# Kernel optimization log

Hardware: AMD Instinct MI355X
Metric: run time of the kernel (lower is better)

## Reference

```python
import jax, jax.numpy as jnp
import numpy as np


def _conv(x, k, pad):
    # x: NHWC, k: HWIO
    return jax.lax.conv_general_dilated(x, k, (1, 1), pad,
                                        dimension_numbers=('NHWC', 'HWIO', 'NHWC'))


def _hard_sigmoid(z):
    return jnp.clip(0.2 * z + 0.5, 0.0, 1.0)


def _convlstm(x_seq, Wx, Wh, b, return_sequences):
    # x_seq: (B,T,H,W,C); Wx: (5,5,C,4F) VALID; Wh: (5,5,F,4F) SAME; b: (4F,)
    B, T, H, W, C = x_seq.shape
    F4 = Wx.shape[-1]
    F = F4 // 4
    # input-to-state convs for all timesteps in one batched conv
    xz = _conv(x_seq.reshape(B * T, H, W, C), Wx, 'VALID') + b
    Ho, Wo = xz.shape[1], xz.shape[2]
    xz = xz.reshape(B, T, Ho, Wo, F4).transpose(1, 0, 2, 3, 4)  # time-major
    h0 = jnp.zeros((B, Ho, Wo, F), x_seq.dtype)
    c0 = h0

    def step(carry, xt):
        h, c = carry
        z = xt + _conv(h, Wh, 'SAME')
        zi, zf, zc, zo = jnp.split(z, 4, axis=-1)  # keras gate order i,f,c,o
        i = _hard_sigmoid(zi)
        f = _hard_sigmoid(zf)
        o = _hard_sigmoid(zo)
        c = f * c + i * jnp.tanh(zc)
        h = o * jnp.tanh(c)
        return (h, c), (h if return_sequences else None)

    (h, c), hs = jax.lax.scan(step, (h0, c0), xz)
    if return_sequences:
        return hs.transpose(1, 0, 2, 3, 4)  # back to (B,T,Ho,Wo,F)
    return h


def setup_inputs() -> dict:
    key = jax.random.key(0)
    ks = jax.random.split(key, 12)
    B, T, H, W, C = 16, 6, 64, 64, 5

    def p(k, shape, scale=0.05):
        return jax.random.normal(k, shape, dtype=jnp.float32) * scale

    x = jax.random.normal(ks[0], (B, T, H, W, C), dtype=jnp.float32)
    # layer1: Cin=5 -> F=128
    Wx1 = p(ks[1], (5, 5, 5, 512));   Wh1 = p(ks[2], (5, 5, 128, 512));  b1 = jnp.zeros((512,), jnp.float32)
    # layer2: Cin=128 -> F=64
    Wx2 = p(ks[3], (5, 5, 128, 256)); Wh2 = p(ks[4], (5, 5, 64, 256));   b2 = jnp.zeros((256,), jnp.float32)
    # layer3: Cin=64 -> F=64
    Wx3 = p(ks[5], (5, 5, 64, 256));  Wh3 = p(ks[6], (5, 5, 64, 256));   b3 = jnp.zeros((256,), jnp.float32)
    D = 52 * 52 * 64  # 173056 after three valid 5x5 convs
    Wd1 = p(ks[7], (D, 1024), 0.01);  bd1 = jnp.zeros((1024,), jnp.float32)
    Wd2 = p(ks[8], (1024, 1024));     bd2 = jnp.zeros((1024,), jnp.float32)
    Wd3 = p(ks[9], (1024, 4));        bd3 = jnp.zeros((4,), jnp.float32)
    return dict(x=x, Wx1=Wx1, Wh1=Wh1, b1=b1, Wx2=Wx2, Wh2=Wh2, b2=b2,
                Wx3=Wx3, Wh3=Wh3, b3=b3, Wd1=Wd1, bd1=bd1, Wd2=Wd2, bd2=bd2,
                Wd3=Wd3, bd3=bd3)


def reference(x, Wx1, Wh1, b1, Wx2, Wh2, b2, Wx3, Wh3, b3,
              Wd1, bd1, Wd2, bd2, Wd3, bd3):
    # NOTE: the original call() computes an average-pool of the input but then
    # overwrites it with conv1(inputs); the pooled branch is dead code.
    h = _convlstm(x, Wx1, Wh1, b1, True)   # (B,T,60,60,128)
    h = _convlstm(h, Wx2, Wh2, b2, True)   # (B,T,56,56,64)
    h = _convlstm(h, Wx3, Wh3, b3, False)  # (B,52,52,64)
    z = h.reshape(h.shape[0], -1)          # keras Flatten = row-major H,W,C
    z = jax.nn.relu(z @ Wd1 + bd1)
    z = jax.nn.relu(z @ Wd2 + bd2)
    return z @ Wd3 + bd3                   # (B,4)
```

## Files before the change

### kernel.cpp

```cpp
#include <hip/hip_runtime.h>

typedef __bf16 bf16;
typedef bf16 bf16x8 __attribute__((ext_vector_type(8)));
typedef float f32x4 __attribute__((ext_vector_type(4)));

__device__ inline bf16x8 bzero8() {
  bf16x8 v;
#pragma unroll
  for (int i = 0; i < 8; ++i) v[i] = (bf16)0.f;
  return v;
}

__device__ __forceinline__ void gload_lds16(const bf16* g, bf16* l) {
  __builtin_amdgcn_global_load_lds(
      (const __attribute__((address_space(1))) void*)g,
      (__attribute__((address_space(3))) void*)l, 16, 0, 0);
}

#define MFMA16 __builtin_amdgcn_mfma_f32_16x16x32_bf16
#define LGKM0 asm volatile("s_waitcnt lgkmcnt(0)")
#define VMC2 asm volatile("s_waitcnt vmcnt(2)")
#define VMC0 asm volatile("s_waitcnt vmcnt(0)")

template <int CIN, int LOG2C>
__global__ void __launch_bounds__(512, 2)
conv_gemm256(const bf16* __restrict__ in, const bf16* __restrict__ wt,
             const float* __restrict__ bias, const bf16* __restrict__ xz,
             bf16* __restrict__ out_bf, float* __restrict__ out_f,
             int HoWo, int Wo, int inH, int inW,
             int T, int t, int N, int K, int epi)
{
  __shared__ bf16 As[2][2][8192];
  __shared__ bf16 Bs[2][2][8192];

  const int tid  = threadIdx.x;
  const int w    = tid >> 6;
  const int lane = tid & 63;

  const int gx  = gridDim.x;
  const int nwg = gx * gridDim.y;
  int flat = blockIdx.y * gx + blockIdx.x;
  {
    const int xcd = flat & 7, o = flat >> 3;
    const int qq = nwg >> 3, rr = nwg & 7;
    flat = (xcd < rr ? xcd * (qq + 1) : rr * (qq + 1) + (xcd - rr) * qq) + o;
  }
  const int n0 = (flat % gx) << 8;
  const int m0 = (flat / gx) << 8;

  const long inHW = (long)inH * inW;
  const int lr8  = lane >> 3;
  const int koff = ((lane & 7) ^ lr8) << 3;

  long baseA[2][2];
  const bf16* wrowp[2][2];
#pragma unroll
  for (int h = 0; h < 2; ++h)
#pragma unroll
    for (int j = 0; j < 2; ++j) {
      const int row = ((j * 8 + w) << 3) + lr8;
      const int gm  = m0 + h * 128 + row;
      const int img = gm / HoWo;
      const int p   = gm - img * HoWo;
      const int ay  = p / Wo;
      const int ax  = p - ay * Wo;
      baseA[h][j] = ((long)img * inHW + (long)ay * inW + ax) << LOG2C;
      wrowp[h][j] = wt + (long)(n0 + h * 128 + row) * K + koff;
    }

  const int KT = K >> 6;

  auto stage = [&](int kt, int half) {
    if (kt >= KT) return;
    const int slot = kt & 1;
    if (half < 2) {
      const int kk = kt << 6;
      const int kc = kk >> LOG2C;
      const int ky = kc / 5;
      const int kx = kc - ky * 5;
      const long toff = ((long)(ky * inW + kx) << LOG2C) + (kk & (CIN - 1)) + koff;
      bf16* d = &As[slot][half][w << 9];
      gload_lds16(in + baseA[half][0] + toff, d);
      gload_lds16(in + baseA[half][1] + toff, d + 4096);
    } else {
      const int h = half - 2;
      bf16* d = &Bs[slot][h][w << 9];
      gload_lds16(wrowp[h][0] + (kt << 6), d);
      gload_lds16(wrowp[h][1] + (kt << 6), d + 4096);
    }
  };

  const int lrow = lane & 15;
  const int lq   = lane >> 4;
  const int wm   = w >> 2;
  const int wn   = w & 3;
  const int s7   = lrow & 7;

  auto rdA = [&](int slot, int r, int ks) -> bf16x8 {
    const int row = (r << 4) + lrow;
    const int ch  = ((ks << 2) + lq) ^ s7;
    return *(const bf16x8*)&As[slot][wm][(row << 6) + (ch << 3)];
  };
  auto rdB = [&](int slot, int cq, int ks) -> bf16x8 {
    const int row = ((wn & 1) << 6) + (cq << 4) + lrow;
    const int ch  = ((ks << 2) + lq) ^ s7;
    return *(const bf16x8*)&Bs[slot][wn >> 1][(row << 6) + (ch << 3)];
  };

  f32x4 acc[8][4];
#pragma unroll
  for (int r = 0; r < 8; ++r)
#pragma unroll
    for (int c = 0; c < 4; ++c) {
      acc[r][c][0] = 0.f; acc[r][c][1] = 0.f;
      acc[r][c][2] = 0.f; acc[r][c][3] = 0.f;
    }

#define QUAD(RB, CB)                                                          \
  __builtin_amdgcn_s_setprio(1);                                              \
  _Pragma("unroll")                                                           \
  for (int r = 0; r < 4; ++r)                                                 \
    _Pragma("unroll")                                                         \
    for (int c = 0; c < 2; ++c) {                                             \
      acc[RB + r][CB + c] =                                                   \
          MFMA16(af[r][0], bq[CB + c][0], acc[RB + r][CB + c], 0, 0, 0);      \
      acc[RB + r][CB + c] =                                                   \
          MFMA16(af[r][1], bq[CB + c][1], acc[RB + r][CB + c], 0, 0, 0);      \
    }                                                                         \
  __builtin_amdgcn_s_setprio(0);

  stage(0, 0); stage(0, 1); stage(0, 2); stage(0, 3);
  stage(1, 0);
  VMC2;
  __builtin_amdgcn_s_barrier();

  bf16x8 af[4][2], bq[4][2];
  const int NI = KT >> 1;
  for (int i = 0; i < NI; ++i) {
    const int t1 = 2 * i + 1, t2 = 2 * i + 2, t3 = 2 * i + 3;
#pragma unroll
    for (int r = 0; r < 4; ++r) { af[r][0] = rdA(0, r, 0); af[r][1] = rdA(0, r, 1); }
#pragma unroll
    for (int c = 0; c < 2; ++c) { bq[c][0] = rdB(0, c, 0); bq[c][1] = rdB(0, c, 1); }
    stage(t1, 1);
    __builtin_amdgcn_s_barrier(); LGKM0;
    QUAD(0, 0)
    __builtin_amdgcn_s_barrier();
#pragma unroll
    for (int c = 2; c < 4; ++c) { bq[c][0] = rdB(0, c, 0); bq[c][1] = rdB(0, c, 1); }
    stage(t1, 2);
    __builtin_amdgcn_s_barrier(); LGKM0;
    QUAD(0, 2)
    __builtin_amdgcn_s_barrier();
#pragma unroll
    for (int r = 0; r < 4; ++r) { af[r][0] = rdA(0, r + 4, 0); af[r][1] = rdA(0, r + 4, 1); }
    stage(t1, 3);
    __builtin_amdgcn_s_barrier(); LGKM0;
    QUAD(4, 2)
    __builtin_amdgcn_s_barrier();
    stage(t2, 0);
    __builtin_amdgcn_s_barrier(); LGKM0;
    QUAD(4, 0)
    if (t2 < KT) { VMC2; } else { VMC0; }
    __builtin_amdgcn_s_barrier();
#pragma unroll
    for (int r = 0; r < 4; ++r) { af[r][0] = rdA(1, r, 0); af[r][1] = rdA(1, r, 1); }
#pragma unroll
    for (int c = 0; c < 2; ++c) { bq[c][0] = rdB(1, c, 0); bq[c][1] = rdB(1, c, 1); }
    stage(t2, 1);
    __builtin_amdgcn_s_barrier(); LGKM0;
    QUAD(0, 0)
    __builtin_amdgcn_s_barrier();
#pragma unroll
    for (int c = 2; c < 4; ++c) { bq[c][0] = rdB(1, c, 0); bq[c][1] = rdB(1, c, 1); }
    stage(t2, 2);
    __builtin_amdgcn_s_barrier(); LGKM0;
    QUAD(0, 2)
    __builtin_amdgcn_s_barrier();
#pragma unroll
    for (int r = 0; r < 4; ++r) { af[r][0] = rdA(1, r + 4, 0); af[r][1] = rdA(1, r + 4, 1); }
    stage(t2, 3);
    __builtin_amdgcn_s_barrier(); LGKM0;
    QUAD(4, 2)
    __builtin_amdgcn_s_barrier();
    stage(t3, 0);
    __builtin_amdgcn_s_barrier(); LGKM0;
    QUAD(4, 0)
    if (t3 < KT) { VMC2; } else { VMC0; }
    __builtin_amdgcn_s_barrier();
  }

  if (KT & 1) {
#pragma unroll
    for (int r = 0; r < 4; ++r) { af[r][0] = rdA(0, r, 0); af[r][1] = rdA(0, r, 1); }
#pragma unroll
    for (int c = 0; c < 4; ++c) { bq[c][0] = rdB(0, c, 0); bq[c][1] = rdB(0, c, 1); }
    QUAD(0, 0)
    QUAD(0, 2)
#pragma unroll
    for (int r = 0; r < 4; ++r) { af[r][0] = rdA(0, r + 4, 0); af[r][1] = rdA(0, r + 4, 1); }
    QUAD(4, 0)
    QUAD(4, 2)
  }
#undef QUAD

  const int colb = n0 + wn * 64 + lrow;
  if (epi == 0) {
    float bsv[4];
#pragma unroll
    for (int c = 0; c < 4; ++c) bsv[c] = bias[colb + c * 16];
#pragma unroll
    for (int r = 0; r < 8; ++r)
#pragma unroll
      for (int q = 0; q < 4; ++q) {
        const long row = m0 + wm * 128 + r * 16 + lq * 4 + q;
#pragma unroll
        for (int c = 0; c < 4; ++c)
          out_bf[row * N + colb + c * 16] = (bf16)(acc[r][c][q] + bsv[c]);
      }
  } else {
#pragma unroll
    for (int r = 0; r < 8; ++r)
#pragma unroll
      for (int q = 0; q < 4; ++q) {
        const int row = m0 + wm * 128 + r * 16 + lq * 4 + q;
        const int b   = row / HoWo;
        const int p   = row - b * HoWo;
        const long xrow = (long)(b * T + t) * HoWo + p;
#pragma unroll
        for (int c = 0; c < 4; ++c) {
          const int nn = colb + c * 16;
          out_f[(long)row * N + nn] = acc[r][c][q] + (float)xz[xrow * N + nn];
        }
      }
  }
}

template <int CIN>
__global__ void __launch_bounds__(256)
conv_gemm64(const bf16* __restrict__ in, const bf16* __restrict__ wt,
            const float* __restrict__ bias, bf16* __restrict__ out_bf,
            int HoWo, int Wo, int inH, int inW, int N, int K)
{
  __shared__ bf16 As[64 * 40];
  __shared__ bf16 Bs[64 * 40];

  const int tid  = threadIdx.x;
  const int wave = tid >> 6;
  const int lane = tid & 63;
  const int m0 = blockIdx.x * 64;
  const int n0 = blockIdx.y * 64;

  const int srow = tid >> 2;
  const int skq  = tid & 3;

  const int am  = m0 + srow;
  const int ab  = am / HoWo;
  const int apx = am - ab * HoWo;
  const int ay  = apx / Wo;
  const int ax  = apx - ay * Wo;
  const long inHW = (long)inH * inW;
  const bf16* inb  = in + (long)ab * inHW * CIN;
  const bf16* wrow = wt + (long)(n0 + srow) * K;

  f32x4 acc[4];
#pragma unroll
  for (int r = 0; r < 4; ++r) { acc[r][0] = 0.f; acc[r][1] = 0.f; acc[r][2] = 0.f; acc[r][3] = 0.f; }

  const int lrow = lane & 15;
  const int lq   = lane >> 4;
  const int ksteps = (K + 31) >> 5;

  for (int ks = 0; ks < ksteps; ++ks) {
    const int k = (ks << 5) + skq * 8;
    bf16x8 av = bzero8(), bv = bzero8();
#pragma unroll
    for (int j = 0; j < 8; ++j) {
      const int ke = k + j;
      if (ke < K) {
        const int c  = ke % CIN;
        const int kc = ke / CIN;
        const int ky = kc / 5;
        const int kx = kc - ky * 5;
        const int iy = ay + ky;
        const int ix = ax + kx;
        av[j] = inb[((long)iy * inW + ix) * CIN + c];
        bv[j] = wrow[ke];
      }
    }
    *(bf16x8*)&As[srow * 40 + skq * 8] = av;
    *(bf16x8*)&Bs[srow * 40 + skq * 8] = bv;
    __syncthreads();

    bf16x8 bfrag = *(const bf16x8*)&Bs[(wave * 16 + lrow) * 40 + lq * 8];
#pragma unroll
    for (int r = 0; r < 4; ++r) {
      bf16x8 afrag = *(const bf16x8*)&As[(r * 16 + lrow) * 40 + lq * 8];
      acc[r] = MFMA16(afrag, bfrag, acc[r], 0, 0, 0);
    }
    __syncthreads();
  }

  const int col = n0 + wave * 16 + lrow;
  const float bsv = bias[col];
#pragma unroll
  for (int r = 0; r < 4; ++r)
#pragma unroll
    for (int q = 0; q < 4; ++q) {
      const long row = m0 + r * 16 + lq * 4 + q;
      out_bf[row * N + col] = (bf16)(acc[r][q] + bsv);
    }
}

__global__ void __launch_bounds__(256)
gate_kernel(const bf16* __restrict__ xz, const float* __restrict__ hz,
            float* __restrict__ c, bf16* __restrict__ hseq,
            bf16* __restrict__ hpad, float* __restrict__ hf,
            int HoWo, int Wo, int Wp, int HpWp, int F, int t, int T, int total)
{
  const int idx = blockIdx.x * 256 + threadIdx.x;
  if (idx >= total) return;
  const int f  = idx % F;
  const int bp = idx / F;
  const int b  = bp / HoWo;
  const int p  = bp - b * HoWo;
  const int N4 = 4 * F;

  float zi, zf, zc, zo;
  if (hz != nullptr) {
    const float* zp = hz + (long)bp * N4 + f;
    zi = zp[0]; zf = zp[F]; zc = zp[2 * F]; zo = zp[3 * F];
  } else {
    const bf16* zp = xz + ((long)(b * T + t) * HoWo + p) * N4 + f;
    zi = (float)zp[0]; zf = (float)zp[F]; zc = (float)zp[2 * F]; zo = (float)zp[3 * F];
  }
  const float cprev = (t > 0) ? c[idx] : 0.f;
  const float ig = fminf(fmaxf(0.2f * zi + 0.5f, 0.f), 1.f);
  const float fg = fminf(fmaxf(0.2f * zf + 0.5f, 0.f), 1.f);
  const float og = fminf(fmaxf(0.2f * zo + 0.5f, 0.f), 1.f);
  const float cn = fg * cprev + ig * tanhf(zc);
  const float h  = og * tanhf(cn);
  c[idx] = cn;
  const bf16 hb = (bf16)h;
  if (hseq != nullptr)
    hseq[((long)(b * T + t) * HoWo + p) * F + f] = hb;
  if (hpad != nullptr) {
    const int y = p / Wo;
    const int x = p - y * Wo;
    hpad[((long)b * HpWp + (long)(y + 2) * Wp + (x + 2)) * F + f] = hb;
  }
  if (hf != nullptr) hf[idx] = h;
}

__global__ void __launch_bounds__(256)
cast_f32_bf16(const float* __restrict__ in, bf16* __restrict__ out, int n)
{
  const int i = blockIdx.x * 256 + threadIdx.x;
  if (i < n) out[i] = (bf16)in[i];
}

__global__ void __launch_bounds__(256)
cast_transpose(const float* __restrict__ in, bf16* __restrict__ out, int K, int N)
{
  const int i = blockIdx.x * 256 + threadIdx.x;
  if (i < K * N) {
    const int k = i / N;
    const int n = i - k * N;
    out[(long)n * K + k] = (bf16)in[i];
  }
}

__global__ void __launch_bounds__(256)
dense_splitk(const float* __restrict__ A, const float* __restrict__ W,
             float* __restrict__ out, int D, int N, int chunk)
{
  const int j  = blockIdx.x * 256 + threadIdx.x;
  const int d0 = blockIdx.y * chunk;
  int d1 = d0 + chunk; if (d1 > D) d1 = D;
  float acc[16];
#pragma unroll
  for (int b = 0; b < 16; ++b) acc[b] = 0.f;
  for (int d = d0; d < d1; ++d) {
    const float w = W[(long)d * N + j];
#pragma unroll
    for (int b = 0; b < 16; ++b) acc[b] += A[(long)b * D + d] * w;
  }
#pragma unroll
  for (int b = 0; b < 16; ++b) atomicAdd(&out[b * N + j], acc[b]);
}

__global__ void __launch_bounds__(256)
bias_relu(const float* __restrict__ in, const float* __restrict__ bias,
          float* __restrict__ out, int N, int total)
{
  const int i = blockIdx.x * 256 + threadIdx.x;
  if (i < total) {
    const int j = i % N;
    const float v = in[i] + bias[j];
    out[i] = v > 0.f ? v : 0.f;
  }
}

__global__ void __launch_bounds__(256)
dense3_kernel(const float* __restrict__ z, const float* __restrict__ W,
              const float* __restrict__ bias, float* __restrict__ out)
{
  const int b = blockIdx.x;
  const int tid = threadIdx.x;
  float a0 = 0.f, a1 = 0.f, a2 = 0.f, a3 = 0.f;
  for (int d = tid; d < 1024; d += 256) {
    const float zv = z[b * 1024 + d];
    a0 += zv * W[d * 4 + 0]; a1 += zv * W[d * 4 + 1];
    a2 += zv * W[d * 4 + 2]; a3 += zv * W[d * 4 + 3];
  }
  __shared__ float red[256][4];
  red[tid][0] = a0; red[tid][1] = a1; red[tid][2] = a2; red[tid][3] = a3;
  __syncthreads();
  for (int s = 128; s > 0; s >>= 1) {
    if (tid < s) {
      red[tid][0] += red[tid + s][0]; red[tid][1] += red[tid + s][1];
      red[tid][2] += red[tid + s][2]; red[tid][3] += red[tid + s][3];
    }
    __syncthreads();
  }
  if (tid < 4) out[b * 4 + tid] = red[0][tid] + bias[tid];
}

extern "C" void kernel_launch(void* const* d_in, const int* in_sizes, int n_in,
                              void* d_out, int out_size, void* d_ws, size_t ws_size,
                              hipStream_t stream)
{
  const float* x   = (const float*)d_in[0];
  const float* Wx1 = (const float*)d_in[1];
  const float* Wh1 = (const float*)d_in[2];
  const float* b1  = (const float*)d_in[3];
  const float* Wx2 = (const float*)d_in[4];
  const float* Wh2 = (const float*)d_in[5];
  const float* b2  = (const float*)d_in[6];
  const float* Wx3 = (const float*)d_in[7];
  const float* Wh3 = (const float*)d_in[8];
  const float* b3  = (const float*)d_in[9];
  const float* Wd1 = (const float*)d_in[10];
  const float* bd1 = (const float*)d_in[11];
  const float* Wd2 = (const float*)d_in[12];
  const float* bd2 = (const float*)d_in[13];
  const float* Wd3 = (const float*)d_in[14];
  const float* bd3 = (const float*)d_in[15];

  char* ws = (char*)d_ws;
  size_t off = 0;
  auto alloc = [&](size_t bytes) -> void* {
    void* p = ws + off;
    off += (bytes + 255) & ~(size_t)255;
    return p;
  };
  bf16* x_bf = (bf16*)alloc((size_t)1966080 * 2);
  bf16* wx1t = (bf16*)alloc((size_t)64000 * 2);
  bf16* wh1t = (bf16*)alloc((size_t)1638400 * 2);
  bf16* wx2t = (bf16*)alloc((size_t)819200 * 2);
  bf16* wh2t = (bf16*)alloc((size_t)409600 * 2);
  bf16* wx3t = (bf16*)alloc((size_t)409600 * 2);
  bf16* wh3t = (bf16*)alloc((size_t)409600 * 2);
  bf16* xzA  = (bf16*)alloc((size_t)176947200 * 2);
  bf16* hB   = (bf16*)alloc((size_t)44236800 * 2);
  float* hzC = (float*)alloc((size_t)29491200 * 4);
  float* cA  = (float*)alloc((size_t)7372800 * 4);
  float* h3f = (float*)alloc((size_t)2768896 * 4);
  bf16* hpadA = (bf16*)alloc((size_t)8388608 * 2);
  float* out1 = (float*)alloc(16384 * 4);
  float* z1   = (float*)alloc(16384 * 4);
  float* out2 = (float*)alloc(16384 * 4);
  float* z2   = (float*)alloc(16384 * 4);

  bf16* h1seq = hB;
  bf16* h2seq = hB;
  float* c1 = cA;
  float* c2 = cA;
  float* c3 = cA + (size_t)3211264;
  bf16* hpad1 = hpadA;
  bf16* hpad2 = hpadA;
  bf16* hpad3 = hpadA + (size_t)3686400;

  cast_f32_bf16<<<(1966080 + 255) / 256, 256, 0, stream>>>(x, x_bf, 1966080);
  cast_transpose<<<(64000 + 255) / 256, 256, 0, stream>>>(Wx1, wx1t, 125, 512);
  cast_transpose<<<(1638400 + 255) / 256, 256, 0, stream>>>(Wh1, wh1t, 3200, 512);
  cast_transpose<<<(819200 + 255) / 256, 256, 0, stream>>>(Wx2, wx2t, 3200, 256);
  cast_transpose<<<(409600 + 255) / 256, 256, 0, stream>>>(Wh2, wh2t, 1600, 256);
  cast_transpose<<<(409600 + 255) / 256, 256, 0, stream>>>(Wx3, wx3t, 1600, 256);
  cast_transpose<<<(409600 + 255) / 256, 256, 0, stream>>>(Wh3, wh3t, 1600, 256);

  hipMemsetAsync(hpadA, 0, (size_t)8388608 * 2, stream);
  conv_gemm64<5><<<dim3(5400, 8), 256, 0, stream>>>(
      x_bf, wx1t, b1, xzA, 3600, 60, 64, 64, 512, 125);
  for (int t = 0; t < 6; ++t) {
    if (t > 0)
      conv_gemm256<128, 7><<<dim3(2, 225), 512, 0, stream>>>(
          hpad1, wh1t, nullptr, xzA, nullptr, hzC,
          3600, 60, 64, 64, 6, t, 512, 3200, 1);
    gate_kernel<<<28800, 256, 0, stream>>>(
        xzA, (t > 0) ? hzC : nullptr, c1, h1seq,
        (t < 5) ? hpad1 : nullptr, nullptr,
        3600, 60, 64, 4096, 128, t, 6, 7372800);
  }

  bf16* xz2 = xzA;
  conv_gemm256<128, 7><<<dim3(1, 1176), 512, 0, stream>>>(
      h1seq, wx2t, b2, nullptr, xz2, nullptr,
      3136, 56, 60, 60, 6, 0, 256, 3200, 0);
  hipMemsetAsync(hpad2, 0, (size_t)3686400 * 2, stream);
  for (int t = 0; t < 6; ++t) {
    if (t > 0)
      conv_gemm256<64, 6><<<dim3(1, 196), 512, 0, stream>>>(
          hpad2, wh2t, nullptr, xz2, nullptr, hzC,
          3136, 56, 60, 60, 6, t, 256, 1600, 1);
    gate_kernel<<<12544, 256, 0, stream>>>(
        xz2, (t > 0) ? hzC : nullptr, c2, h2seq,
        (t < 5) ? hpad2 : nullptr, nullptr,
        3136, 56, 60, 3600, 64, t, 6, 3211264);
  }

  bf16* xz3 = xzA;
  conv_gemm256<64, 6><<<dim3(1, 1014), 512, 0, stream>>>(
      h2seq, wx3t, b3, nullptr, xz3, nullptr,
      2704, 52, 56, 56, 6, 0, 256, 1600, 0);
  hipMemsetAsync(hpad3, 0, (size_t)3211264 * 2, stream);
  for (int t = 0; t < 6; ++t) {
    if (t > 0)
      conv_gemm256<64, 6><<<dim3(1, 169), 512, 0, stream>>>(
          hpad3, wh3t, nullptr, xz3, nullptr, hzC,
          2704, 52, 56, 56, 6, t, 256, 1600, 1);
    gate_kernel<<<10816, 256, 0, stream>>>(
        xz3, (t > 0) ? hzC : nullptr, c3, nullptr,
        (t < 5) ? hpad3 : nullptr, (t == 5) ? h3f : nullptr,
        2704, 52, 56, 3136, 64, t, 6, 2768896);
  }

  hipMemsetAsync(out1, 0, 16384 * 4, stream);
  hipMemsetAsync(out2, 0, 16384 * 4, stream);
  dense_splitk<<<dim3(4, 169), 256, 0, stream>>>(h3f, Wd1, out1, 173056, 1024, 1024);
  bias_relu<<<64, 256, 0, stream>>>(out1, bd1, z1, 1024, 16384);
  dense_splitk<<<dim3(4, 4), 256, 0, stream>>>(z1, Wd2, out2, 1024, 1024, 256);
  bias_relu<<<64, 256, 0, stream>>>(out2, bd2, z2, 1024, 16384);
  dense3_kernel<<<16, 256, 0, stream>>>(z2, Wd3, bd3, (float*)d_out);
}
```

Measured before the change: 4.687 ms.

## Replace atomic split-K dense layers with partial-sum buffers and fused bias-ReLU reduction

The dense layers move from a split-K kernel using float atomics into a two-stage scheme. First, 256 blocks each cover a D-chunk for all 1024 outputs, using 4-wide vectorized weight loads, and write partial sums to a buffer. A second kernel reduces those partials and fuses in the bias add and ReLU, which removes the memsets and atomics. This changes the work split of the large Wd1 GEMV (about 708 MB of fp32 weights) so it spreads over more blocks, at the cost of extra partial-buffer traffic and higher per-thread register use from 64 accumulators.

```diff
diff --git a/kernel.cpp b/kernel.cpp
--- a/kernel.cpp
+++ b/kernel.cpp
@@ -371,34 +371,50 @@
 }
 
 __global__ void __launch_bounds__(256)
-dense_splitk(const float* __restrict__ A, const float* __restrict__ W,
-             float* __restrict__ out, int D, int N, int chunk)
-{
-  const int j  = blockIdx.x * 256 + threadIdx.x;
-  const int d0 = blockIdx.y * chunk;
+dense_stage1(const float* __restrict__ A, const float* __restrict__ W,
+             float* __restrict__ part, int D, int chunk)
+{
+  const int tid = threadIdx.x;
+  const int j4  = tid << 2;
+  const int g   = blockIdx.x;
+  const int d0  = g * chunk;
   int d1 = d0 + chunk; if (d1 > D) d1 = D;
-  float acc[16];
-#pragma unroll
-  for (int b = 0; b < 16; ++b) acc[b] = 0.f;
-  for (int d = d0; d < d1; ++d) {
-    const float w = W[(long)d * N + j];
-#pragma unroll
-    for (int b = 0; b < 16; ++b) acc[b] += A[(long)b * D + d] * w;
-  }
-#pragma unroll
-  for (int b = 0; b < 16; ++b) atomicAdd(&out[b * N + j], acc[b]);
-}
-
-__global__ void __launch_bounds__(256)
-bias_relu(const float* __restrict__ in, const float* __restrict__ bias,
-          float* __restrict__ out, int N, int total)
+
+  f32x4 acc[16];
+#pragma unroll
+  for (int b = 0; b < 16; ++b) {
+    acc[b][0] = 0.f; acc[b][1] = 0.f; acc[b][2] = 0.f; acc[b][3] = 0.f;
+  }
+
+  for (int d = d0; d < d1; d += 4) {
+#pragma unroll
+    for (int u = 0; u < 4; ++u) {
+      const f32x4 w4 = *(const f32x4*)&W[(long)(d + u) * 1024 + j4];
+#pragma unroll
+      for (int b = 0; b < 16; ++b) {
+        const float a = A[(long)b * D + d + u];
+        acc[b][0] += a * w4[0]; acc[b][1] += a * w4[1];
+        acc[b][2] += a * w4[2]; acc[b][3] += a * w4[3];
+      }
+    }
+  }
+
+  float* po = part + ((long)g << 14);
+#pragma unroll
+  for (int b = 0; b < 16; ++b)
+    *(f32x4*)&po[(b << 10) + j4] = acc[b];
+}
+
+__global__ void __launch_bounds__(256)
+dense_reduce(const float* __restrict__ part, const float* __restrict__ bias,
+             float* __restrict__ out, int G)
 {
   const int i = blockIdx.x * 256 + threadIdx.x;
-  if (i < total) {
-    const int j = i % N;
-    const float v = in[i] + bias[j];
-    out[i] = v > 0.f ? v : 0.f;
-  }
+  const int j = i & 1023;
+  float s = bias[j];
+#pragma unroll 4
+  for (int g = 0; g < G; ++g) s += part[((long)g << 14) + i];
+  out[i] = s > 0.f ? s : 0.f;
 }
 
 __global__ void __launch_bounds__(256)
@@ -467,9 +483,8 @@
   float* cA  = (float*)alloc((size_t)7372800 * 4);
   float* h3f = (float*)alloc((size_t)2768896 * 4);
   bf16* hpadA = (bf16*)alloc((size_t)8388608 * 2);
-  float* out1 = (float*)alloc(16384 * 4);
+  float* part = (float*)alloc((size_t)256 * 16384 * 4);
   float* z1   = (float*)alloc(16384 * 4);
-  float* out2 = (float*)alloc(16384 * 4);
   float* z2   = (float*)alloc(16384 * 4);
 
   bf16* h1seq = hB;
@@ -535,11 +550,9 @@
         2704, 52, 56, 3136, 64, t, 6, 2768896);
   }
 
-  hipMemsetAsync(out1, 0, 16384 * 4, stream);
-  hipMemsetAsync(out2, 0, 16384 * 4, stream);
-  dense_splitk<<<dim3(4, 169), 256, 0, stream>>>(h3f, Wd1, out1, 173056, 1024, 1024);
-  bias_relu<<<64, 256, 0, stream>>>(out1, bd1, z1, 1024, 16384);
-  dense_splitk<<<dim3(4, 4), 256, 0, stream>>>(z1, Wd2, out2, 1024, 1024, 256);
-  bias_relu<<<64, 256, 0, stream>>>(out2, bd2, z2, 1024, 16384);
+  dense_stage1<<<256, 256, 0, stream>>>(h3f, Wd1, part, 173056, 676);
+  dense_reduce<<<64, 256, 0, stream>>>(part, bd1, z1, 256);
+  dense_stage1<<<16, 256, 0, stream>>>(z1, Wd2, part, 1024, 64);
+  dense_reduce<<<64, 256, 0, stream>>>(part, bd2, z2, 16);
   dense3_kernel<<<16, 256, 0, stream>>>(z2, Wd3, bd3, (float*)d_out);
 }
```

New measurement: 4.390 ms. 1.07x faster.
